# Kernel tuning notes

Hardware: AMD Instinct MI355X
Metric: run time of the kernel (lower is better)

## Reference

```python
import jax, jax.numpy as jnp
import numpy as np
from jax import lax

R = 3
D = (2 * R + 1) ** 2  # 49 local offsets


def _unfold(x, r):
    # torch F.unfold(kernel=2r+1, padding=r): (B,C,H,W) -> (B, C*K*K, H, W),
    # channel-major (c, ky, kx) ordering, matching conv_general_dilated_patches.
    k = 2 * r + 1
    return lax.conv_general_dilated_patches(
        x, (k, k), (1, 1), [(r, r), (r, r)],
        dimension_numbers=("NCHW", "OIHW", "NCHW"))


def _l2norm(x, eps=1e-12):
    n = jnp.sqrt(jnp.sum(x * x, axis=1, keepdims=True))
    return x / jnp.maximum(n, eps)


def setup_inputs() -> dict:
    key = jax.random.key(0)
    ks = jax.random.split(key, 8)
    B, Cin, Cmid, H, W = 2, 256, 128, 112, 112
    phi_cur = jax.random.normal(ks[0], (B, Cin, H, W), jnp.float32)
    phi_rnd = jax.random.normal(ks[1], (B, Cin, H, W), jnp.float32)
    P_cur = jax.random.normal(ks[2], (B, 3, H, W), jnp.float32)
    P_rnd = jax.random.normal(ks[3], (B, 3, H, W), jnp.float32)
    Wq = jax.random.normal(ks[4], (Cmid, Cin), jnp.float32) * 0.05
    Wk = jax.random.normal(ks[5], (Cmid, Cin), jnp.float32) * 0.05
    Wv = jax.random.normal(ks[6], (D, D), jnp.float32) * 0.1
    bv = jnp.zeros((D,), jnp.float32)
    gamma = jnp.array(1.0, jnp.float32)
    return dict(phi_cur=phi_cur, phi_rnd=phi_rnd, P_cur=P_cur, P_rnd=P_rnd,
                Wq=Wq, Wk=Wk, Wv=Wv, bv=bv, gamma=gamma)


def reference(phi_cur, phi_rnd, P_cur, P_rnd, Wq, Wk, Wv, bv, gamma):
    B, _, H, W = phi_cur.shape
    # 1x1 convs + channel L2 normalize
    q = _l2norm(jnp.einsum('oc,bchw->bohw', Wq, phi_cur))
    k = _l2norm(jnp.einsum('oc,bchw->bohw', Wk, phi_rnd))
    # local cost volume: patches (B, Cmid, D, H, W)
    patches = _unfold(k, R).reshape(B, -1, D, H, W)
    corr = jnp.einsum('bchw,bcdhw->bdhw', q, patches)  # (B,D,H,W)
    vol_corr = jnp.einsum('ed,bdhw->behw', Wv, corr) + bv[None, :, None, None]
    # geometric bias
    Pr = _unfold(P_rnd, R).reshape(B, 3, D, H, W)
    dP = P_cur[:, :, None, :, :] - Pr  # (B,3,D,H,W)
    dz = dP[:, 2]
    dist = jnp.sqrt(jnp.clip(jnp.sum(dP * dP, axis=1), 1e-12, None))
    logits = vol_corr + gamma * (-dist - 0.5 * jnp.abs(dz))
    w = jax.nn.softmax(logits, axis=1)
    off = jnp.arange(-R, R + 1, dtype=w.dtype)
    dY, dX = jnp.meshgrid(off, off, indexing='ij')
    offx = dX.reshape(1, D, 1, 1)
    offy = dY.reshape(1, D, 1, 1)
    du = jnp.sum(w * offx, axis=1, keepdims=True)
    dv = jnp.sum(w * offy, axis=1, keepdims=True)
    conf = jnp.max(w, axis=1, keepdims=True)
    return du, dv, conf
```

## Files before the change

### kernel.cpp

```cpp
#include <hip/hip_runtime.h>
#include <math.h>

constexpr int B    = 2;
constexpr int CIN  = 256;
constexpr int CMID = 128;
constexpr int H    = 112;
constexpr int W    = 112;
constexpr int HW   = H * W;
constexpr int NPIX = B * HW;
constexpr int RAD  = 3;
constexpr int KS   = 7;
constexpr int DD   = 49;

typedef __attribute__((ext_vector_type(8))) short  short8;
typedef __attribute__((ext_vector_type(4))) float  float4v;

__device__ __forceinline__ unsigned short f2bf(float f) {
    unsigned u = __float_as_uint(f);
    u += 0x7FFFu + ((u >> 16) & 1u);
    return (unsigned short)(u >> 16);
}
__device__ __forceinline__ unsigned pkbf(float a, float b) {
    return (unsigned)f2bf(a) | ((unsigned)f2bf(b) << 16);
}

__global__ __launch_bounds__(256) void convert_w(
    const float* __restrict__ Wq, const float* __restrict__ Wk,
    unsigned short* __restrict__ wqb, unsigned short* __restrict__ wkb)
{
    const int i  = blockIdx.x * 256 + threadIdx.x;
    const int n4 = (CMID * CIN) / 4;
    const float4 v = (i < n4) ? ((const float4*)Wq)[i] : ((const float4*)Wk)[i - n4];
    uint2 r;
    r.x = pkbf(v.x, v.y);
    r.y = pkbf(v.z, v.w);
    if (i < n4) ((uint2*)wqb)[i] = r;
    else        ((uint2*)wkb)[i - n4] = r;
}

constexpr int PSTR = 264;

__global__ __launch_bounds__(256) void proj_mfma(
    const float* __restrict__ phi_cur, const float* __restrict__ phi_rnd,
    const unsigned short* __restrict__ wq_bf, const unsigned short* __restrict__ wk_bf,
    unsigned short* __restrict__ q_ws, unsigned short* __restrict__ k_ws)
{
    __shared__ unsigned short pt[64 * PSTR];
    __shared__ float red[4][64];

    const int tid  = threadIdx.x;
    const int lane = tid & 63;
    const int wv   = __builtin_amdgcn_readfirstlane(tid >> 6);
    const int t    = blockIdx.y;

    const float* __restrict__ phi          = t ? phi_rnd : phi_cur;
    const unsigned short* __restrict__ Wbf = t ? wk_bf : wq_bf;
    unsigned short* __restrict__ outp      = t ? k_ws : q_ws;

    const int pgb = blockIdx.x * 64;
    const int b   = pgb / HW;
    const int pim = pgb % HW;
    const float* pbase = phi + (size_t)b * CIN * HW + pim;

#pragma unroll
    for (int pass = 0; pass < 8; ++pass) {
        const int idx = pass * 256 + tid;
        const int cp  = idx >> 4;
        const int pq  = idx & 15;
        const int c0  = cp * 2;
        const float4 va = *(const float4*)(pbase + (size_t)c0 * HW + pq * 4);
        const float4 vb = *(const float4*)(pbase + (size_t)(c0 + 1) * HW + pq * 4);
        *(unsigned*)(pt + (pq * 4 + 0) * PSTR + c0) = pkbf(va.x, vb.x);
        *(unsigned*)(pt + (pq * 4 + 1) * PSTR + c0) = pkbf(va.y, vb.y);
        *(unsigned*)(pt + (pq * 4 + 2) * PSTR + c0) = pkbf(va.z, vb.z);
        *(unsigned*)(pt + (pq * 4 + 3) * PSTR + c0) = pkbf(va.w, vb.w);
    }

    const int m = lane & 15, quad = lane >> 4;
    short8 af[2][8];
#pragma unroll
    for (int ot = 0; ot < 2; ++ot)
#pragma unroll
        for (int kc = 0; kc < 8; ++kc)
            af[ot][kc] = *(const short8*)(Wbf +
                (size_t)(wv * 32 + ot * 16 + m) * CIN + kc * 32 + quad * 8);

    __syncthreads();

    float4v acc[2][4];
#pragma unroll
    for (int ot = 0; ot < 2; ++ot)
#pragma unroll
        for (int nt = 0; nt < 4; ++nt) acc[ot][nt] = (float4v)0.f;

#pragma unroll
    for (int kc = 0; kc < 8; ++kc) {
        short8 bf[4];
#pragma unroll
        for (int nt = 0; nt < 4; ++nt)
            bf[nt] = *(const short8*)(pt + (nt * 16 + m) * PSTR + kc * 32 + quad * 8);
#pragma unroll
        for (int ot = 0; ot < 2; ++ot)
#pragma unroll
            for (int nt = 0; nt < 4; ++nt)
                acc[ot][nt] = __builtin_amdgcn_mfma_f32_16x16x32_bf16(
                    af[ot][kc], bf[nt], acc[ot][nt], 0, 0, 0);
    }

#pragma unroll
    for (int nt = 0; nt < 4; ++nt) {
        float ss = 0.f;
#pragma unroll
        for (int ot = 0; ot < 2; ++ot)
#pragma unroll
            for (int r = 0; r < 4; ++r)
                ss = fmaf(acc[ot][nt][r], acc[ot][nt][r], ss);
        ss += __shfl_xor(ss, 16, 64);
        ss += __shfl_xor(ss, 32, 64);
        if (quad == 0) red[wv][nt * 16 + m] = ss;
    }
    __syncthreads();

    float inv[4];
#pragma unroll
    for (int nt = 0; nt < 4; ++nt) {
        const int px = nt * 16 + m;
        const float tot = red[0][px] + red[1][px] + red[2][px] + red[3][px];
        inv[nt] = 1.f / fmaxf(sqrtf(tot), 1e-12f);
    }

#pragma unroll
    for (int nt = 0; nt < 4; ++nt)
#pragma unroll
        for (int ot = 0; ot < 2; ++ot) {
            uint2 st;
            st.x = pkbf(acc[ot][nt][0] * inv[nt], acc[ot][nt][1] * inv[nt]);
            st.y = pkbf(acc[ot][nt][2] * inv[nt], acc[ot][nt][3] * inv[nt]);
            *(uint2*)(outp + (size_t)(pgb + nt * 16 + m) * CMID
                      + wv * 32 + ot * 16 + quad * 4) = st;
        }
}

constexpr int TILE = 16;
constexpr int COLS = TILE + 6;
constexpr int NV   = KS * COLS;
constexpr int KSTR = 136;

__global__ __launch_bounds__(256) void corr_kernel(
    const unsigned short* __restrict__ q_ws, const unsigned short* __restrict__ k_ws,
    const float* __restrict__ P_cur, const float* __restrict__ P_rnd,
    const float* __restrict__ Wvm, const float* __restrict__ bv,
    const float* __restrict__ gamma_p, float* __restrict__ out)
{
    __shared__ unsigned short kt[NV * KSTR];
    __shared__ unsigned short qt[TILE * KSTR];
    __shared__ float cs[TILE][52];

    const int tid  = threadIdx.x;
    const int lane = tid & 63;
    const int wv   = __builtin_amdgcn_readfirstlane(tid >> 6);
    const int w0   = blockIdx.x * TILE;
    const int h    = blockIdx.y;
    const int b    = blockIdx.z;

    const int sub  = tid & 15;
    const int vgrp = tid >> 4;
#pragma unroll
    for (int pass = 0; pass < 10; ++pass) {
        const int vi = pass * 16 + vgrp;
        if (vi < NV) {
            const int rr = vi / COLS;
            const int cc = vi % COLS;
            const int hh = h + rr - RAD;
            const int ww = w0 + cc - RAD;
            uint4 v = make_uint4(0, 0, 0, 0);
            if (hh >= 0 && hh < H && ww >= 0 && ww < W)
                v = *(const uint4*)(k_ws + (size_t)(b * HW + hh * W + ww) * CMID + sub * 8);
            *(uint4*)(kt + vi * KSTR + sub * 8) = v;
        }
    }
    {
        const uint4 v = *(const uint4*)(q_ws + (size_t)(b * HW + h * W + w0 + vgrp) * CMID + sub * 8);
        *(uint4*)(qt + vgrp * KSTR + sub * 8) = v;
    }

    const int  ld    = (lane < DD) ? lane : 0;
    const bool valid = (lane < DD);
    float wrow[52];
#pragma unroll
    for (int e = 0; e < DD; ++e) wrow[e] = Wvm[ld * DD + e];
    wrow[49] = wrow[50] = wrow[51] = 0.f;
    const float bvv   = bv[ld];
    const float gamma = gamma_p[0];

    __syncthreads();

    if (tid < TILE * 3)
        cs[tid / 3][49 + tid % 3] = 0.f;

    const int m = lane & 15, quad = lane >> 4;
    for (int g = wv; g < 14; g += 4) {
        const int r  = g >> 1;
        const int nt = g & 1;
        const int vi = min(r * COLS + nt * 16 + m, NV - 1);
        float4v acc = (float4v)0.f;
#pragma unroll
        for (int kc = 0; kc < 4; ++kc) {
            const short8 afrag = *(const short8*)(qt + m * KSTR + kc * 32 + quad * 8);
            const short8 bfrag = *(const short8*)(kt + vi * KSTR + kc * 32 + quad * 8);
            acc = __builtin_amdgcn_mfma_f32_16x16x32_bf16(afrag, bfrag, acc, 0, 0, 0);
        }
#pragma unroll
        for (int reg = 0; reg < 4; ++reg) {
            const int p   = quad * 4 + reg;
            const int off = nt * 16 + m - p;
            if (off >= 0 && off <= 6)
                cs[p][r * 7 + off] = acc[reg];
        }
    }
    __syncthreads();

    const int dy = ld / KS - RAD;
    const int dx = ld % KS - RAD;

    for (int i = 0; i < 4; ++i) {
        const int pl = wv * 4 + i;
        const int pg = b * HW + h * W + w0 + pl;

        const int hn = h + dy, wn = w0 + pl + dx;
        const bool inb = valid && hn >= 0 && hn < H && wn >= 0 && wn < W;
        const float* pc = P_cur + (size_t)b * 3 * HW + (h * W + w0 + pl);
        const float cx = pc[0], cy = pc[HW], cz = pc[2 * HW];
        float rx = 0.f, ry = 0.f, rz = 0.f;
        if (inb) {
            const float* pr = P_rnd + (size_t)b * 3 * HW + (hn * W + wn);
            rx = pr[0]; ry = pr[HW]; rz = pr[2 * HW];
        }
        const float dpx = cx - rx, dpy = cy - ry, dpz = cz - rz;
        const float dist = sqrtf(fmaxf(dpx * dpx + dpy * dpy + dpz * dpz, 1e-12f));

        float logit = -INFINITY;
        if (valid) {
            float v = bvv;
#pragma unroll
            for (int e4 = 0; e4 < 13; ++e4) {
                const float4 c4 = *(const float4*)&cs[pl][e4 * 4];
                v = fmaf(wrow[e4 * 4 + 0], c4.x, v);
                v = fmaf(wrow[e4 * 4 + 1], c4.y, v);
                v = fmaf(wrow[e4 * 4 + 2], c4.z, v);
                v = fmaf(wrow[e4 * 4 + 3], c4.w, v);
            }
            logit = v + gamma * (-dist - 0.5f * fabsf(dpz));
        }

        float lmax = logit;
#pragma unroll
        for (int off = 32; off; off >>= 1)
            lmax = fmaxf(lmax, __shfl_xor(lmax, off, 64));
        const float e1 = valid ? __expf(logit - lmax) : 0.f;
        float Z = e1;
#pragma unroll
        for (int off = 32; off; off >>= 1)
            Z += __shfl_xor(Z, off, 64);
        const float wgt = e1 / Z;

        float dus = wgt * (float)dx;
        float dvs = wgt * (float)dy;
#pragma unroll
        for (int off = 32; off; off >>= 1) {
            dus += __shfl_xor(dus, off, 64);
            dvs += __shfl_xor(dvs, off, 64);
        }

        if (lane == 0) {
            out[pg]            = dus;
            out[NPIX + pg]     = dvs;
            out[2 * NPIX + pg] = 1.f / Z;
        }
    }
}

extern "C" void kernel_launch(void* const* d_in, const int* in_sizes, int n_in,
                              void* d_out, int out_size, void* d_ws, size_t ws_size,
                              hipStream_t stream)
{
    const float* phi_cur = (const float*)d_in[0];
    const float* phi_rnd = (const float*)d_in[1];
    const float* P_cur   = (const float*)d_in[2];
    const float* P_rnd   = (const float*)d_in[3];
    const float* Wq      = (const float*)d_in[4];
    const float* Wk      = (const float*)d_in[5];
    const float* Wv      = (const float*)d_in[6];
    const float* bv      = (const float*)d_in[7];
    const float* gm      = (const float*)d_in[8];
    float* out = (float*)d_out;

    unsigned short* ws   = (unsigned short*)d_ws;
    unsigned short* q_ws = ws;
    unsigned short* k_ws = q_ws + (size_t)NPIX * CMID;
    unsigned short* wqb  = k_ws + (size_t)NPIX * CMID;
    unsigned short* wkb  = wqb + (size_t)CMID * CIN;

    convert_w<<<dim3(2 * CMID * CIN / 4 / 256), 256, 0, stream>>>(Wq, Wk, wqb, wkb);

    proj_mfma<<<dim3(NPIX / 64, 2), 256, 0, stream>>>(
        phi_cur, phi_rnd, wqb, wkb, q_ws, k_ws);

    corr_kernel<<<dim3(W / TILE, H, B), 256, 0, stream>>>(
        q_ws, k_ws, P_cur, P_rnd, Wv, bv, gm, out);
}
```

Before: 143.1 us.

## Fuse weight bf16 conversion into projection and batch softmax reductions via LDS

```diff
diff --git a/kernel.cpp b/kernel.cpp
--- a/kernel.cpp
+++ b/kernel.cpp
@@ -1,4 +1,5 @@
 #include <hip/hip_runtime.h>
+#include <hip/hip_bf16.h>
 #include <math.h>
 
 constexpr int B    = 2;
@@ -15,34 +16,18 @@
 typedef __attribute__((ext_vector_type(8))) short  short8;
 typedef __attribute__((ext_vector_type(4))) float  float4v;
 
-__device__ __forceinline__ unsigned short f2bf(float f) {
-    unsigned u = __float_as_uint(f);
-    u += 0x7FFFu + ((u >> 16) & 1u);
-    return (unsigned short)(u >> 16);
-}
 __device__ __forceinline__ unsigned pkbf(float a, float b) {
-    return (unsigned)f2bf(a) | ((unsigned)f2bf(b) << 16);
-}
-
-__global__ __launch_bounds__(256) void convert_w(
-    const float* __restrict__ Wq, const float* __restrict__ Wk,
-    unsigned short* __restrict__ wqb, unsigned short* __restrict__ wkb)
-{
-    const int i  = blockIdx.x * 256 + threadIdx.x;
-    const int n4 = (CMID * CIN) / 4;
-    const float4 v = (i < n4) ? ((const float4*)Wq)[i] : ((const float4*)Wk)[i - n4];
-    uint2 r;
-    r.x = pkbf(v.x, v.y);
-    r.y = pkbf(v.z, v.w);
-    if (i < n4) ((uint2*)wqb)[i] = r;
-    else        ((uint2*)wkb)[i - n4] = r;
+    __hip_bfloat162 h = __float22bfloat162_rn(make_float2(a, b));
+    union { __hip_bfloat162 h2; unsigned u; } c;
+    c.h2 = h;
+    return c.u;
 }
 
 constexpr int PSTR = 264;
 
 __global__ __launch_bounds__(256) void proj_mfma(
     const float* __restrict__ phi_cur, const float* __restrict__ phi_rnd,
-    const unsigned short* __restrict__ wq_bf, const unsigned short* __restrict__ wk_bf,
+    const float* __restrict__ Wq, const float* __restrict__ Wk,
     unsigned short* __restrict__ q_ws, unsigned short* __restrict__ k_ws)
 {
     __shared__ unsigned short pt[64 * PSTR];
@@ -53,9 +38,9 @@
     const int wv   = __builtin_amdgcn_readfirstlane(tid >> 6);
     const int t    = blockIdx.y;
 
-    const float* __restrict__ phi          = t ? phi_rnd : phi_cur;
-    const unsigned short* __restrict__ Wbf = t ? wk_bf : wq_bf;
-    unsigned short* __restrict__ outp      = t ? k_ws : q_ws;
+    const float* __restrict__ phi  = t ? phi_rnd : phi_cur;
+    const float* __restrict__ Wf   = t ? Wk : Wq;
+    unsigned short* __restrict__ outp = t ? k_ws : q_ws;
 
     const int pgb = blockIdx.x * 64;
     const int b   = pgb / HW;
@@ -81,9 +66,18 @@
 #pragma unroll
     for (int ot = 0; ot < 2; ++ot)
 #pragma unroll
-        for (int kc = 0; kc < 8; ++kc)
-            af[ot][kc] = *(const short8*)(Wbf +
-                (size_t)(wv * 32 + ot * 16 + m) * CIN + kc * 32 + quad * 8);
+        for (int kc = 0; kc < 8; ++kc) {
+            const float* wr = Wf + (size_t)(wv * 32 + ot * 16 + m) * CIN
+                                 + kc * 32 + quad * 8;
+            const float4 w0 = *(const float4*)(wr);
+            const float4 w1 = *(const float4*)(wr + 4);
+            union { short8 s; unsigned u[4]; } cv;
+            cv.u[0] = pkbf(w0.x, w0.y);
+            cv.u[1] = pkbf(w0.z, w0.w);
+            cv.u[2] = pkbf(w1.x, w1.y);
+            cv.u[3] = pkbf(w1.z, w1.w);
+            af[ot][kc] = cv.s;
+        }
 
     __syncthreads();
 
@@ -153,7 +147,7 @@
     const float* __restrict__ gamma_p, float* __restrict__ out)
 {
     __shared__ unsigned short kt[NV * KSTR];
-    __shared__ unsigned short qt[TILE * KSTR];
+    __shared__ alignas(16) unsigned short qt[TILE * KSTR];
     __shared__ float cs[TILE][52];
 
     const int tid  = threadIdx.x;
@@ -219,13 +213,14 @@
         }
     }
     __syncthreads();
+    float* lsf = reinterpret_cast<float*>(qt);
 
     const int dy = ld / KS - RAD;
     const int dx = ld % KS - RAD;
 
+#pragma unroll
     for (int i = 0; i < 4; ++i) {
         const int pl = wv * 4 + i;
-        const int pg = b * HW + h * W + w0 + pl;
 
         const int hn = h + dy, wn = w0 + pl + dx;
         const bool inb = valid && hn >= 0 && hn < H && wn >= 0 && wn < W;
@@ -252,30 +247,51 @@
             }
             logit = v + gamma * (-dist - 0.5f * fabsf(dpz));
         }
-
-        float lmax = logit;
-#pragma unroll
-        for (int off = 32; off; off >>= 1)
-            lmax = fmaxf(lmax, __shfl_xor(lmax, off, 64));
-        const float e1 = valid ? __expf(logit - lmax) : 0.f;
-        float Z = e1;
-#pragma unroll
-        for (int off = 32; off; off >>= 1)
-            Z += __shfl_xor(Z, off, 64);
-        const float wgt = e1 / Z;
-
-        float dus = wgt * (float)dx;
-        float dvs = wgt * (float)dy;
-#pragma unroll
-        for (int off = 32; off; off >>= 1) {
-            dus += __shfl_xor(dus, off, 64);
-            dvs += __shfl_xor(dvs, off, 64);
-        }
-
-        if (lane == 0) {
-            out[pg]            = dus;
-            out[NPIX + pg]     = dvs;
-            out[2 * NPIX + pg] = 1.f / Z;
+        lsf[pl * 64 + lane] = logit;
+    }
+
+    {
+        const int pli = lane >> 4;
+        const int dq  = lane & 15;
+        const int pl  = wv * 4 + pli;
+
+        const float4 v = ((const float4*)lsf)[pl * 16 + dq];
+
+        float m4 = fmaxf(fmaxf(v.x, v.y), fmaxf(v.z, v.w));
+#pragma unroll
+        for (int s = 1; s < 16; s <<= 1)
+            m4 = fmaxf(m4, __shfl_xor(m4, s, 64));
+
+        const float e0 = __expf(v.x - m4);
+        const float e1 = __expf(v.y - m4);
+        const float e2 = __expf(v.z - m4);
+        const float e3 = __expf(v.w - m4);
+        float Z = (e0 + e1) + (e2 + e3);
+
+        const int c0i = dq * 4;
+        float dus = 0.f, dvs = 0.f;
+        {
+            const float ex[4] = { e0, e1, e2, e3 };
+#pragma unroll
+            for (int j = 0; j < 4; ++j) {
+                const int col = c0i + j;
+                dus = fmaf(ex[j], (float)(col % KS - RAD), dus);
+                dvs = fmaf(ex[j], (float)(col / KS - RAD), dvs);
+            }
+        }
+#pragma unroll
+        for (int s = 1; s < 16; s <<= 1) {
+            Z   += __shfl_xor(Z,   s, 64);
+            dus += __shfl_xor(dus, s, 64);
+            dvs += __shfl_xor(dvs, s, 64);
+        }
+
+        if (dq == 0) {
+            const int pg = b * HW + h * W + w0 + pl;
+            const float invZ = 1.f / Z;
+            out[pg]            = dus * invZ;
+            out[NPIX + pg]     = dvs * invZ;
+            out[2 * NPIX + pg] = invZ;
         }
     }
 }
@@ -298,13 +314,9 @@
     unsigned short* ws   = (unsigned short*)d_ws;
     unsigned short* q_ws = ws;
     unsigned short* k_ws = q_ws + (size_t)NPIX * CMID;
-    unsigned short* wqb  = k_ws + (size_t)NPIX * CMID;
-    unsigned short* wkb  = wqb + (size_t)CMID * CIN;
-
-    convert_w<<<dim3(2 * CMID * CIN / 4 / 256), 256, 0, stream>>>(Wq, Wk, wqb, wkb);
 
     proj_mfma<<<dim3(NPIX / 64, 2), 256, 0, stream>>>(
-        phi_cur, phi_rnd, wqb, wkb, q_ws, k_ws);
+        phi_cur, phi_rnd, Wq, Wk, q_ws, k_ws);
 
     corr_kernel<<<dim3(W / TILE, H, B), 256, 0, stream>>>(
         q_ws, k_ws, P_cur, P_rnd, Wv, bv, gm, out);
```

Result: no change. 141.5 us (-1.2%).
